# Kernel optimization log

Hardware: AMD Instinct MI355X
Metric: run time of the kernel (lower is better)

The kernel has to match this reference:

```python
import jax, jax.numpy as jnp
import numpy as np

B, D, C, E, K = 4096, 784, 10, 1024, 8   # batch, input_size, num_classes, num_classifiers, k_neighbors
TANH_FACTOR = 10.0
EPS = 1e-12


def setup_inputs() -> dict:
    key = jax.random.key(0)
    ks = jax.random.split(key, 8)
    x = jax.random.normal(ks[0], (B, D), dtype=jnp.float32)
    keys_raw = jax.random.normal(ks[1], (E, D), dtype=jnp.float32)
    keys = keys_raw / jnp.maximum(jnp.linalg.norm(keys_raw, axis=1, keepdims=True), EPS)
    # weak-learner weights (VarianceScaling fan_in ~ 1/sqrt(D)) and biases
    Wm = jax.random.normal(ks[2], (E, C, D), dtype=jnp.float32) / jnp.sqrt(D)
    bm = jnp.zeros((E, C), dtype=jnp.float32)
    # vanilla classifier (scale=0.1 -> std ~ sqrt(0.1/D))
    Wv = jax.random.normal(ks[3], (C, D), dtype=jnp.float32) * jnp.sqrt(0.1 / D)
    bv = jnp.zeros((C,), dtype=jnp.float32)
    # tanh classifier
    Wt = jax.random.normal(ks[4], (C, D), dtype=jnp.float32) * jnp.sqrt(0.1 / D)
    bt = jnp.zeros((C,), dtype=jnp.float32)
    return {"x": x, "keys": keys, "Wm": Wm, "bm": bm, "Wv": Wv, "bv": bv, "Wt": Wt, "bt": bt}


def reference(x, keys, Wm, bm, Wv, bv, Wt, bt):
    # --- lookup_memory: cosine-similarity routing (keys are pre-normalized) ---
    xn = x / jnp.maximum(jnp.linalg.norm(x, axis=1, keepdims=True), EPS)  # l2 normalize
    cos = xn @ keys.T                       # [B, E]
    sims, idx = jax.lax.top_k(cos, K)       # descending similarity, [B, K]
    # Faithful to torch: experts are gathered in ascending model-index order
    # (enumerate over ModuleList), while weights `sims` stay similarity-sorted.
    gidx = jnp.sort(idx, axis=1)            # [B, K]

    # --- ensemble_forward: gather expert weights, per-sample tiny GEMVs ---
    Wg = Wm[gidx]                           # [B, K, C, D] (irregular gather)
    bg = bm[gidx]                           # [B, K, C]
    expert_raw = jnp.einsum('bd,bkcd->bkc', x, Wg) + bg
    expert_out = jnp.tanh(expert_raw / TANH_FACTOR) * TANH_FACTOR
    w = sims[..., None]                     # [B, K, 1]
    ensemble = jnp.sum(expert_out * w, axis=1) / jnp.sum(w, axis=1)  # [B, C]

    # --- vanilla / tanh classifiers ---
    vanilla = jax.nn.log_softmax(x @ Wv.T + bv, axis=1)
    tanh_out = jnp.tanh((x @ Wt.T + bt) / TANH_FACTOR) * TANH_FACTOR
    return ensemble, tanh_out, vanilla
```

## Files before the change

### kernel.cpp

```cpp
#include <hip/hip_runtime.h>
#include <hip/hip_bf16.h>
#include <math.h>

#define B_ 4096
#define D_ 784
#define C_ 10
#define E_ 1024
#define K_ 8
#define KP 832
#define CHR 104
#define NW 1088
#define LDR 72
#define LDW 840
#define CAP 48
#define ECAP 128
#define MARG 0.04f

typedef float f32x4 __attribute__((ext_vector_type(4)));
typedef short s16x8 __attribute__((ext_vector_type(8)));

__device__ __forceinline__ float wave_reduce_sum(float v) {
  #pragma unroll
  for (int off = 32; off > 0; off >>= 1) v += __shfl_xor(v, off, 64);
  return v;
}

__device__ __forceinline__ float bitonic64_f(float v, int lane) {
  #pragma unroll
  for (int k = 2; k <= 64; k <<= 1)
    #pragma unroll
    for (int j = k >> 1; j > 0; j >>= 1) {
      float o = __shfl_xor(v, j, 64);
      bool keepmin = ((lane & j) == 0) == ((lane & k) == 0);
      v = keepmin ? fminf(v, o) : fmaxf(v, o);
    }
  return v;
}

__device__ __forceinline__ unsigned long long bitonic64_u(unsigned long long v, int lane) {
  #pragma unroll
  for (int k = 2; k <= 64; k <<= 1)
    #pragma unroll
    for (int j = k >> 1; j > 0; j >>= 1) {
      unsigned long long o = __shfl_xor(v, j, 64);
      bool keepmin = ((lane & j) == 0) == ((lane & k) == 0);
      v = keepmin ? (v < o ? v : o) : (v < o ? o : v);
    }
  return v;
}

__device__ __forceinline__ unsigned long long packkey(float v, int idx) {
  unsigned ub = __float_as_uint(v);
  ub = (ub & 0x80000000u) ? ~ub : (ub | 0x80000000u);
  return ((unsigned long long)ub << 32) | (unsigned)(~idx);
}
__device__ __forceinline__ float unpackval(unsigned long long k) {
  unsigned ub = (unsigned)(k >> 32);
  unsigned fb = (ub & 0x80000000u) ? (ub ^ 0x80000000u) : ~ub;
  return __uint_as_float(fb);
}

__global__ __launch_bounds__(256) void prep_all(const float* __restrict__ x,
                                                const float* __restrict__ keys,
                                                const float* __restrict__ Wv,
                                                const float* __restrict__ Wt,
                                                unsigned short* __restrict__ xh,
                                                unsigned short* __restrict__ kh,
                                                float* __restrict__ out_ens,
                                                int* __restrict__ count) {
  int gt = blockIdx.x * 256 + threadIdx.x;
  if (gt < E_) count[gt] = 0;
  int t = gt;
  const float* src = nullptr;
  unsigned short* dst;
  if (t < B_ * CHR) {
    int row = t / CHR, ch = t % CHR;
    dst = xh + (size_t)row * KP + ch * 8;
    src = (ch < 98) ? x + (size_t)row * D_ + ch * 8 : nullptr;
  } else {
    t -= B_ * CHR;
    if (t < NW * CHR) {
      int row = t / CHR, ch = t % CHR;
      dst = kh + (size_t)row * KP + ch * 8;
      if (ch < 98) {
        if (row < E_) src = keys + (size_t)row * D_ + ch * 8;
        else if (row < E_ + 10) src = Wv + (size_t)(row - E_) * D_ + ch * 8;
        else if (row < E_ + 20) src = Wt + (size_t)(row - E_ - 10) * D_ + ch * 8;
      }
    } else {
      t -= NW * CHR;
      if (t < (B_ * C_) / 4) {
        float4 z = make_float4(0.f, 0.f, 0.f, 0.f);
        ((float4*)out_ens)[t] = z;
      }
      return;
    }
  }
  unsigned short u[8];
  if (src) {
    #pragma unroll
    for (int i = 0; i < 8; ++i) {
      __hip_bfloat16 h = __float2bfloat16(src[i]);
      u[i] = *(unsigned short*)&h;
    }
  } else {
    #pragma unroll
    for (int i = 0; i < 8; ++i) u[i] = 0;
  }
  *(uint4*)dst = *(uint4*)u;
}

__global__ __launch_bounds__(256) void gemm_bf16(const unsigned short* __restrict__ xh,
                                                 const unsigned short* __restrict__ kh,
                                                 float* __restrict__ cosb) {
  __shared__ unsigned short As[64 * LDR];
  __shared__ unsigned short Bs[64 * LDR];
  const int tid  = threadIdx.x;
  const int bid  = blockIdx.y * 17 + blockIdx.x;
  const int swz  = (bid & 7) * 136 + (bid >> 3);
  const int row0 = (swz / 17) * 64, col0 = (swz % 17) * 64;
  const int srow = tid >> 2, sq = tid & 3;
  const int lane = tid & 63, w = tid >> 6;
  const int wr = (w >> 1) * 32, wc = (w & 1) * 32;
  const int fr = lane & 15, fg = lane >> 4;

  const unsigned short* gx = xh + (size_t)(row0 + srow) * KP;
  const unsigned short* gk = kh + (size_t)(col0 + srow) * KP;
  unsigned short* sa = As + srow * LDR + sq * 8;
  unsigned short* sb = Bs + srow * LDR + sq * 8;
  const unsigned short* pa0 = As + (wr + fr) * LDR + fg * 8;
  const unsigned short* pb0 = Bs + (wc + fr) * LDR + fg * 8;

  uint4 va0 = *(const uint4*)(gx + sq * 8);
  uint4 va1 = *(const uint4*)(gx + 32 + sq * 8);
  uint4 vb0 = *(const uint4*)(gk + sq * 8);
  uint4 vb1 = *(const uint4*)(gk + 32 + sq * 8);

  f32x4 acc[2][2] = {};
  for (int t = 0; t < 13; ++t) {
    __syncthreads();
    *(uint4*)sa = va0; *(uint4*)(sa + 32) = va1;
    *(uint4*)sb = vb0; *(uint4*)(sb + 32) = vb1;
    __syncthreads();
    if (t < 12) {
      int k1 = (t + 1) * 64;
      va0 = *(const uint4*)(gx + k1 + sq * 8);
      va1 = *(const uint4*)(gx + k1 + 32 + sq * 8);
      vb0 = *(const uint4*)(gk + k1 + sq * 8);
      vb1 = *(const uint4*)(gk + k1 + 32 + sq * 8);
    }
    #pragma unroll
    for (int kk = 0; kk < 64; kk += 32) {
      s16x8 a0 = *(const s16x8*)(pa0 + kk);
      s16x8 a1 = *(const s16x8*)(pa0 + 16 * LDR + kk);
      s16x8 b0 = *(const s16x8*)(pb0 + kk);
      s16x8 b1 = *(const s16x8*)(pb0 + 16 * LDR + kk);
      acc[0][0] = __builtin_amdgcn_mfma_f32_16x16x32_bf16(a0, b0, acc[0][0], 0, 0, 0);
      acc[0][1] = __builtin_amdgcn_mfma_f32_16x16x32_bf16(a0, b1, acc[0][1], 0, 0, 0);
      acc[1][0] = __builtin_amdgcn_mfma_f32_16x16x32_bf16(a1, b0, acc[1][0], 0, 0, 0);
      acc[1][1] = __builtin_amdgcn_mfma_f32_16x16x32_bf16(a1, b1, acc[1][1], 0, 0, 0);
    }
  }
  #pragma unroll
  for (int m = 0; m < 2; ++m)
    #pragma unroll
    for (int n = 0; n < 2; ++n)
      #pragma unroll
      for (int j = 0; j < 4; ++j) {
        int r = row0 + wr + m * 16 + fg * 4 + j;
        int c = col0 + wc + n * 16 + fr;
        cosb[(size_t)r * NW + c] = acc[m][n][j];
      }
}

__global__ __launch_bounds__(256) void topk_select(const float* __restrict__ cosb,
                                                   const float* __restrict__ x,
                                                   const float* __restrict__ keys,
                                                   const float* __restrict__ bv,
                                                   const float* __restrict__ bt,
                                                   float* __restrict__ sims,
                                                   int* __restrict__ count,
                                                   int* __restrict__ list,
                                                   float* __restrict__ out_tanh,
                                                   float* __restrict__ out_van) {
  __shared__ unsigned long long sKey[4][CAP];
  const int tid = threadIdx.x, w = tid >> 6, lane = tid & 63;
  const int row = (blockIdx.x << 2) + w;
  const float* cr = cosb + (size_t)row * NW;

  {
    float hv = (lane < 20) ? cr[E_ + lane] : 0.f;
    float vv = 0.f, tv = 0.f;
    if (lane < 10) vv = hv + bv[lane];
    else if (lane < 20) tv = hv + bt[lane - 10];
    float mv = (lane < 10) ? vv : -__builtin_inff();
    #pragma unroll
    for (int off = 1; off < 16; off <<= 1) mv = fmaxf(mv, __shfl_xor(mv, off, 64));
    float ev = (lane < 10) ? expf(vv - mv) : 0.f;
    float se = ev;
    #pragma unroll
    for (int off = 1; off < 16; off <<= 1) se += __shfl_xor(se, off, 64);
    if (lane < 10) out_van[(size_t)row * C_ + lane] = vv - (mv + logf(se));
    else if (lane < 20) out_tanh[(size_t)row * C_ + (lane - 10)] = tanhf(tv * 0.1f) * 10.0f;
  }

  float vals[16];
  #pragma unroll
  for (int j = 0; j < 16; ++j) vals[j] = cr[j * 64 + lane];
  float lm = vals[0];
  #pragma unroll
  for (int j = 1; j < 16; ++j) lm = fmaxf(lm, vals[j]);

  float srt = bitonic64_f(lm, lane);
  const float thr = __shfl(srt, 56) - MARG;

  int cnt = 0;
  #pragma unroll
  for (int j = 0; j < 16; ++j) {
    bool p = vals[j] >= thr;
    unsigned long long mk = __ballot(p);
    if (p) {
      int pos = cnt + __popcll(mk & ((1ull << lane) - 1ull));
      if (pos < CAP) sKey[w][pos] = packkey(vals[j], j * 64 + lane);
    }
    cnt += __popcll(mk);
  }
  const int m = cnt < CAP ? cnt : CAP;

  unsigned long long key = (lane < m) ? sKey[w][lane] : 0ull;
  key = bitonic64_u(key, lane);

  const float a8 = unpackval(__shfl(key, 56));
  const float a9 = unpackval(__shfl(key, 55));

  if (a8 - a9 <= MARG) {
    const float4* xp4 = (const float4*)(x + (size_t)row * D_);
    float4 xr[4];
    #pragma unroll
    for (int i = 0; i < 3; ++i) xr[i] = xp4[i * 64 + lane];
    xr[3] = make_float4(0.f, 0.f, 0.f, 0.f);
    if (lane < 4) xr[3] = xp4[192 + lane];

    float myv = unpackval(key);
    unsigned long long rm = __ballot(key != 0ull && fabsf(myv - a8) <= MARG);
    while (rm) {
      int L = __builtin_ctzll(rm);
      rm &= rm - 1;
      unsigned long long kL = __shfl(key, L);
      int ei = (int)(~(unsigned)kL) & (E_ - 1);
      const float4* kp4 = (const float4*)(keys + (size_t)ei * D_);
      float s = 0.f;
      #pragma unroll
      for (int i = 0; i < 3; ++i) {
        float4 kv = kp4[i * 64 + lane];
        s += xr[i].x * kv.x + xr[i].y * kv.y + xr[i].z * kv.z + xr[i].w * kv.w;
      }
      if (lane < 4) {
        float4 kv = kp4[192 + lane];
        s += xr[3].x * kv.x + xr[3].y * kv.y + xr[3].z * kv.z + xr[3].w * kv.w;
      }
      s = wave_reduce_sum(s);
      if (lane == L) key = packkey(s, ei);
    }
    key = bitonic64_u(key, lane);
  }

  if (lane >= 56) {
    float simv = unpackval(key);
    int ei = (int)(~(unsigned)key) & (E_ - 1);
    float ssum = simv;
    ssum += __shfl_xor(ssum, 1, 64);
    ssum += __shfl_xor(ssum, 2, 64);
    ssum += __shfl_xor(ssum, 4, 64);
    sims[row * K_ + (63 - lane)] = simv / ssum;
    int si = ei;
    const int l3 = lane & 7;
    #pragma unroll
    for (int k = 2; k <= 8; k <<= 1) {
      #pragma unroll
      for (int j = k >> 1; j > 0; j >>= 1) {
        int o = __shfl_xor(si, j, 64);
        bool lower = (l3 & j) == 0;
        bool asc = (l3 & k) == 0;
        int mn = si < o ? si : o;
        int mx = si < o ? o : si;
        si = (lower == asc) ? mn : mx;
      }
    }
    int pos = atomicAdd(&count[si], 1);
    if (pos < ECAP) list[si * ECAP + pos] = row * K_ + (lane - 56);
  }
}

__global__ __launch_bounds__(256) void expert_mfma(const float* __restrict__ Wm,
                                                   const float* __restrict__ bm,
                                                   const unsigned short* __restrict__ xh,
                                                   const int* __restrict__ list,
                                                   const int* __restrict__ count,
                                                   const float* __restrict__ sims,
                                                   float* __restrict__ out_ens) {
  __shared__ unsigned short Wl[16 * LDW];
  const int e   = blockIdx.x;
  const int tid = threadIdx.x;
  int n = count[e];
  n = n < ECAP ? n : ECAP;
  const int base = e * ECAP;

  for (int ch = tid; ch < 16 * CHR; ch += 256) {
    int r  = ch / CHR;
    int kc = (ch % CHR) * 8;
    unsigned short u[8];
    if (r < 10 && kc < 784) {
      const float4* s4 = (const float4*)(Wm + (size_t)e * (C_ * D_) + r * D_ + kc);
      float4 f0 = s4[0], f1 = s4[1];
      __hip_bfloat16 h;
      h = __float2bfloat16(f0.x); u[0] = *(unsigned short*)&h;
      h = __float2bfloat16(f0.y); u[1] = *(unsigned short*)&h;
      h = __float2bfloat16(f0.z); u[2] = *(unsigned short*)&h;
      h = __float2bfloat16(f0.w); u[3] = *(unsigned short*)&h;
      h = __float2bfloat16(f1.x); u[4] = *(unsigned short*)&h;
      h = __float2bfloat16(f1.y); u[5] = *(unsigned short*)&h;
      h = __float2bfloat16(f1.z); u[6] = *(unsigned short*)&h;
      h = __float2bfloat16(f1.w); u[7] = *(unsigned short*)&h;
    } else {
      #pragma unroll
      for (int i = 0; i < 8; ++i) u[i] = 0;
    }
    *(uint4*)(Wl + r * LDW + kc) = *(uint4*)u;
  }
  __syncthreads();
  if (n == 0) return;

  const int lane = tid & 63, w = tid >> 6;
  const int fr = lane & 15, fg = lane >> 4;
  const float bias = (fr < C_) ? bm[e * C_ + fr] : 0.f;
  const unsigned short* bp = Wl + fr * LDW + fg * 8;

  for (int c0 = w * 16; c0 < n; c0 += 64) {
    int sidx = c0 + fr;
    int item = (sidx < n) ? list[base + sidx] : list[base];
    const unsigned short* xrow = xh + (size_t)(item >> 3) * KP + fg * 8;
    f32x4 acc = {};
    #pragma unroll
    for (int k0 = 0; k0 < KP; k0 += 32) {
      s16x8 a = *(const s16x8*)(xrow + k0);
      s16x8 b = *(const s16x8*)(bp + k0);
      acc = __builtin_amdgcn_mfma_f32_16x16x32_bf16(a, b, acc, 0, 0, 0);
    }
    if (fr < C_) {
      #pragma unroll
      for (int j = 0; j < 4; ++j) {
        int s2 = c0 + fg * 4 + j;
        if (s2 < n) {
          int it2 = list[base + s2];
          float sc = sims[it2];
          float val = tanhf((acc[j] + bias) * 0.1f) * 10.0f;
          atomicAdd(&out_ens[(size_t)(it2 >> 3) * C_ + fr], val * sc);
        }
      }
    }
  }
}

extern "C" void kernel_launch(void* const* d_in, const int* in_sizes, int n_in,
                              void* d_out, int out_size, void* d_ws, size_t ws_size,
                              hipStream_t stream) {
  const float* x    = (const float*)d_in[0];
  const float* keys = (const float*)d_in[1];
  const float* Wm   = (const float*)d_in[2];
  const float* bm   = (const float*)d_in[3];
  const float* Wv   = (const float*)d_in[4];
  const float* bv   = (const float*)d_in[5];
  const float* Wt   = (const float*)d_in[6];
  const float* bt   = (const float*)d_in[7];
  float* out = (float*)d_out;
  float* out_ens  = out;
  float* out_tanh = out + (size_t)B_ * C_;
  float* out_van  = out + 2 * (size_t)B_ * C_;

  char* p = (char*)d_ws;
  auto carve = [&](size_t bytes) { char* q = p; p += (bytes + 255) & ~(size_t)255; return q; };
  float* cosb  = (float*)carve((size_t)B_ * NW * 4);
  float* sims  = (float*)carve(B_ * K_ * 4);
  unsigned short* xh = (unsigned short*)carve((size_t)B_ * KP * 2);
  unsigned short* kh = (unsigned short*)carve((size_t)NW * KP * 2);
  int*   count  = (int*)carve(E_ * 4);
  int*   list   = (int*)carve((size_t)E_ * ECAP * 4);

  int prep_threads = B_ * CHR + NW * CHR + (B_ * C_) / 4;
  prep_all<<<(prep_threads + 255) / 256, 256, 0, stream>>>(x, keys, Wv, Wt, xh, kh,
                                                           out_ens, count);
  dim3 g(NW / 64, B_ / 64);
  gemm_bf16<<<g, 256, 0, stream>>>(xh, kh, cosb);
  topk_select<<<B_ / 4, 256, 0, stream>>>(cosb, x, keys, bv, bt, sims, count, list,
                                          out_tanh, out_van);
  expert_mfma<<<E_, 256, 0, stream>>>(Wm, bm, xh, list, count, sims, out_ens);
}
```

Measured before the change: 80.72 us.

## Double-buffer GEMM tiles with direct global-to-LDS loads and XOR swizzle

Rewrites the bf16 cosine GEMM main loop so tiles go straight from global memory into LDS via global_load_lds, rather than staging through registers. Shared memory becomes two buffers, so the next K tile is issued while MFMAs run on the current one, and the loop drops to one barrier per iteration. The padded row stride is replaced by an XOR swizzle of the 16-byte chunks to avoid LDS bank conflicts. Correctness depends on the async LDS loads being complete before the barrier, which relies on the compiler inserting the right waitcnt.

Result: slower. 84.52 us (+4.7%).

```diff
diff --git a/kernel.cpp b/kernel.cpp
--- a/kernel.cpp
+++ b/kernel.cpp
@@ -10,7 +10,6 @@
 #define KP 832
 #define CHR 104
 #define NW 1088
-#define LDR 72
 #define LDW 840
 #define CAP 48
 #define ECAP 128
@@ -58,6 +57,12 @@
   unsigned ub = (unsigned)(k >> 32);
   unsigned fb = (ub & 0x80000000u) ? (ub ^ 0x80000000u) : ~ub;
   return __uint_as_float(fb);
+}
+
+__device__ __forceinline__ void gload16(const unsigned short* g, unsigned short* l) {
+  __builtin_amdgcn_global_load_lds(
+      (const __attribute__((address_space(1))) unsigned int*)g,
+      (__attribute__((address_space(3))) unsigned int*)l, 16, 0, 0);
 }
 
 __global__ __launch_bounds__(256) void prep_all(const float* __restrict__ x,
@@ -113,54 +118,61 @@
 __global__ __launch_bounds__(256) void gemm_bf16(const unsigned short* __restrict__ xh,
                                                  const unsigned short* __restrict__ kh,
                                                  float* __restrict__ cosb) {
-  __shared__ unsigned short As[64 * LDR];
-  __shared__ unsigned short Bs[64 * LDR];
+  __shared__ unsigned short As[2][64 * 64];
+  __shared__ unsigned short Bs[2][64 * 64];
   const int tid  = threadIdx.x;
   const int bid  = blockIdx.y * 17 + blockIdx.x;
   const int swz  = (bid & 7) * 136 + (bid >> 3);
   const int row0 = (swz / 17) * 64, col0 = (swz % 17) * 64;
-  const int srow = tid >> 2, sq = tid & 3;
   const int lane = tid & 63, w = tid >> 6;
   const int wr = (w >> 1) * 32, wc = (w & 1) * 32;
   const int fr = lane & 15, fg = lane >> 4;
 
-  const unsigned short* gx = xh + (size_t)(row0 + srow) * KP;
-  const unsigned short* gk = kh + (size_t)(col0 + srow) * KP;
-  unsigned short* sa = As + srow * LDR + sq * 8;
-  unsigned short* sb = Bs + srow * LDR + sq * 8;
-  const unsigned short* pa0 = As + (wr + fr) * LDR + fg * 8;
-  const unsigned short* pb0 = Bs + (wc + fr) * LDR + fg * 8;
-
-  uint4 va0 = *(const uint4*)(gx + sq * 8);
-  uint4 va1 = *(const uint4*)(gx + 32 + sq * 8);
-  uint4 vb0 = *(const uint4*)(gk + sq * 8);
-  uint4 vb1 = *(const uint4*)(gk + 32 + sq * 8);
+  const int sr  = w * 16 + (lane >> 3);
+  const int scg = (lane & 7) ^ (sr & 7);
+  const unsigned short* gA0 = xh + (size_t)(row0 + sr) * KP + scg * 8;
+  const unsigned short* gA1 = xh + (size_t)(row0 + sr + 8) * KP + scg * 8;
+  const unsigned short* gB0 = kh + (size_t)(col0 + sr) * KP + scg * 8;
+  const unsigned short* gB1 = kh + (size_t)(col0 + sr + 8) * KP + scg * 8;
+
+  #define ISSUE(buf, k0) {                                   \
+    gload16(gA0 + (k0), &As[buf][(w * 16) * 64]);            \
+    gload16(gA1 + (k0), &As[buf][(w * 16 + 8) * 64]);        \
+    gload16(gB0 + (k0), &Bs[buf][(w * 16) * 64]);            \
+    gload16(gB1 + (k0), &Bs[buf][(w * 16 + 8) * 64]); }
+
+  const int sl0 = (fg ^ (fr & 7)) * 8;
+  const int sl1 = ((fg ^ (fr & 7)) ^ 4) * 8;
 
   f32x4 acc[2][2] = {};
+  ISSUE(0, 0);
+  __syncthreads();
   for (int t = 0; t < 13; ++t) {
+    if (t < 12) ISSUE((t + 1) & 1, (t + 1) * 64);
+    const int b = t & 1;
+    const unsigned short* pa0 = &As[b][(wr + fr) * 64];
+    const unsigned short* pa1 = &As[b][(wr + 16 + fr) * 64];
+    const unsigned short* pb0 = &Bs[b][(wc + fr) * 64];
+    const unsigned short* pb1 = &Bs[b][(wc + 16 + fr) * 64];
+    s16x8 a0 = *(const s16x8*)(pa0 + sl0);
+    s16x8 a1 = *(const s16x8*)(pa1 + sl0);
+    s16x8 b0 = *(const s16x8*)(pb0 + sl0);
+    s16x8 b1 = *(const s16x8*)(pb1 + sl0);
+    acc[0][0] = __builtin_amdgcn_mfma_f32_16x16x32_bf16(a0, b0, acc[0][0], 0, 0, 0);
+    acc[0][1] = __builtin_amdgcn_mfma_f32_16x16x32_bf16(a0, b1, acc[0][1], 0, 0, 0);
+    acc[1][0] = __builtin_amdgcn_mfma_f32_16x16x32_bf16(a1, b0, acc[1][0], 0, 0, 0);
+    acc[1][1] = __builtin_amdgcn_mfma_f32_16x16x32_bf16(a1, b1, acc[1][1], 0, 0, 0);
+    s16x8 a2 = *(const s16x8*)(pa0 + sl1);
+    s16x8 a3 = *(const s16x8*)(pa1 + sl1);
+    s16x8 b2 = *(const s16x8*)(pb0 + sl1);
+    s16x8 b3 = *(const s16x8*)(pb1 + sl1);
+    acc[0][0] = __builtin_amdgcn_mfma_f32_16x16x32_bf16(a2, b2, acc[0][0], 0, 0, 0);
+    acc[0][1] = __builtin_amdgcn_mfma_f32_16x16x32_bf16(a2, b3, acc[0][1], 0, 0, 0);
+    acc[1][0] = __builtin_amdgcn_mfma_f32_16x16x32_bf16(a3, b2, acc[1][0], 0, 0, 0);
+    acc[1][1] = __builtin_amdgcn_mfma_f32_16x16x32_bf16(a3, b3, acc[1][1], 0, 0, 0);
     __syncthreads();
-    *(uint4*)sa = va0; *(uint4*)(sa + 32) = va1;
-    *(uint4*)sb = vb0; *(uint4*)(sb + 32) = vb1;
-    __syncthreads();
-    if (t < 12) {
-      int k1 = (t + 1) * 64;
-      va0 = *(const uint4*)(gx + k1 + sq * 8);
-      va1 = *(const uint4*)(gx + k1 + 32 + sq * 8);
-      vb0 = *(const uint4*)(gk + k1 + sq * 8);
-      vb1 = *(const uint4*)(gk + k1 + 32 + sq * 8);
-    }
-    #pragma unroll
-    for (int kk = 0; kk < 64; kk += 32) {
-      s16x8 a0 = *(const s16x8*)(pa0 + kk);
-      s16x8 a1 = *(const s16x8*)(pa0 + 16 * LDR + kk);
-      s16x8 b0 = *(const s16x8*)(pb0 + kk);
-      s16x8 b1 = *(const s16x8*)(pb0 + 16 * LDR + kk);
-      acc[0][0] = __builtin_amdgcn_mfma_f32_16x16x32_bf16(a0, b0, acc[0][0], 0, 0, 0);
-      acc[0][1] = __builtin_amdgcn_mfma_f32_16x16x32_bf16(a0, b1, acc[0][1], 0, 0, 0);
-      acc[1][0] = __builtin_amdgcn_mfma_f32_16x16x32_bf16(a1, b0, acc[1][0], 0, 0, 0);
-      acc[1][1] = __builtin_amdgcn_mfma_f32_16x16x32_bf16(a1, b1, acc[1][1], 0, 0, 0);
-    }
-  }
+  }
+  #undef ISSUE
   #pragma unroll
   for (int m = 0; m < 2; ++m)
     #pragma unroll
```
